# Optimization experiments

Hardware: AMD Instinct MI355X
Metric: run time of the kernel (lower is better)

Reference implementation:

```python
import jax, jax.numpy as jnp
import numpy as np


def setup_inputs() -> dict:
    key = jax.random.key(0)
    k0, k1, k2, k3, k4 = jax.random.split(key, 5)
    N, C, H, W, K = 16, 256, 32, 32, 4096
    inv = 1.0 / np.sqrt(C).astype(np.float32)
    latent = jax.random.normal(k0, (N, C, H, W), jnp.float32)
    codebook = jax.random.normal(k1, (K, C), jnp.float32) * inv
    wq = jax.random.normal(k2, (C, C), jnp.float32) * inv
    wk = jax.random.normal(k3, (C, C), jnp.float32) * inv
    wv = jax.random.normal(k4, (C, C), jnp.float32) * inv
    return {"latent": latent, "codebook": codebook, "wq": wq, "wk": wk, "wv": wv, "temperature": 1}


def reference(latent, codebook, wq, wk, wv, temperature):
    # deterministic=True, additionWeight=True, dropout=False
    # temperature >= 0 -> _gumbelAttention -> _softStraightThrough path
    assert temperature >= 0
    C = latent.shape[1]
    K = codebook.shape[0]
    scale = jnp.sqrt(jnp.asarray(C, jnp.float32))
    x = jnp.transpose(latent, (0, 2, 3, 1))          # [N,H,W,C]
    q = x @ wq.T                                      # nn.Linear: x @ W^T
    k = codebook @ wk.T                               # [K,C]
    v = codebook @ wv.T                               # [K,C]
    logit = jnp.einsum('nhwc,kc->nhwk', q, k) / scale  # [N,H,W,K]
    soft = jax.nn.softmax(logit, axis=-1)
    idx = jnp.argmax(logit, axis=-1)                  # [N,H,W]
    hard = jax.nn.one_hot(idx, K, dtype=jnp.float32)  # [N,H,W,K]
    soft_v = jnp.einsum('nhwk,kc->nhwc', soft, v)
    hard_v = jnp.einsum('nhwk,kc->nhwc', hard, v)
    # (hard - soft).detach() + soft  -> straight-through estimator
    result = jax.lax.stop_gradient(hard_v - soft_v) + soft_v
    quantized = jnp.transpose(result, (0, 3, 1, 2))   # [N,C,H,W]
    code = idx.astype(jnp.uint8)                      # sample.argmax(-1).byte()
    return (quantized, code, logit, v)
```

## Files before the change

kernel.cpp:

```cpp
#include <hip/hip_runtime.h>
#include <stdint.h>

typedef float f32x4 __attribute__((ext_vector_type(4)));
typedef short s16x8 __attribute__((ext_vector_type(8)));

#define QUANT_OFF 0
#define CODE_OFF  4194304
#define LOGIT_OFF 4210688
#define V_OFF     71319552

#define ARGMAX_MARGIN 0.0078125f

__device__ __forceinline__ unsigned short f2bf(float f) {
  unsigned int u = __float_as_uint(f);
  u = u + 0x7fffu + ((u >> 16) & 1u);
  return (unsigned short)(u >> 16);
}

__device__ __forceinline__ void load_lds16(const void* g, void* l) {
  __builtin_amdgcn_global_load_lds(
      (const __attribute__((address_space(1))) unsigned int*)g,
      (__attribute__((address_space(3))) unsigned int*)l, 16, 0, 0);
}

__global__ __launch_bounds__(256) void kvq_kernel(
    const float* __restrict__ latent, const float* __restrict__ wq,
    const float* __restrict__ cb, const float* __restrict__ wk, const float* __restrict__ wv,
    float* __restrict__ qf, unsigned short* __restrict__ qh,
    float* __restrict__ kf, unsigned short* __restrict__ kh, float* __restrict__ vout)
{
  __shared__ __align__(16) float As[64][68];
  __shared__ __align__(16) float Bs[64][68];
  const int t = threadIdx.x;
  const int bid = blockIdx.x;
  const int tx = t & 15;
  const int ry = t >> 4;

  if (bid >= 256) {
    const int qb = bid - 256;
    const int rowBase = (qb & 255) * 64;
    const int colBase = (qb >> 8) * 64;
    const int n = rowBase >> 10;
    const int hw0 = rowBase & 1023;
    const f32x4* lat4 = (const f32x4*)latent;
    const f32x4* wq4 = (const f32x4*)wq;
    float acc[4][4] = {{0.f}};
    for (int kt = 0; kt < 4; ++kt) {
      __syncthreads();
      #pragma unroll
      for (int it = 0; it < 4; ++it) {
        int c = it * 256 + t;
        int kk = c >> 4, rq = c & 15;
        f32x4 vv = lat4[(size_t)(n * 256 + kt * 64 + kk) * 256 + (hw0 >> 2) + rq];
        *(f32x4*)&As[kk][rq * 4] = vv;
      }
      #pragma unroll
      for (int it = 0; it < 4; ++it) {
        int c = it * 256 + t;
        int col = c >> 4, kq4 = c & 15;
        f32x4 vv = wq4[(size_t)(colBase + col) * 64 + kt * 16 + kq4];
        *(f32x4*)&Bs[col][kq4 * 4] = vv;
      }
      __syncthreads();
      #pragma unroll
      for (int kc = 0; kc < 16; ++kc) {
        f32x4 a[4], b[4];
        #pragma unroll
        for (int c = 0; c < 4; ++c) a[c] = *(const f32x4*)&As[kc * 4 + c][ry * 4];
        #pragma unroll
        for (int j = 0; j < 4; ++j) b[j] = *(const f32x4*)&Bs[tx + 16 * j][kc * 4];
        #pragma unroll
        for (int i = 0; i < 4; ++i)
          #pragma unroll
          for (int j = 0; j < 4; ++j) {
            acc[i][j] = fmaf(a[0][i], b[j].x, acc[i][j]);
            acc[i][j] = fmaf(a[1][i], b[j].y, acc[i][j]);
            acc[i][j] = fmaf(a[2][i], b[j].z, acc[i][j]);
            acc[i][j] = fmaf(a[3][i], b[j].w, acc[i][j]);
          }
      }
    }
    #pragma unroll
    for (int i = 0; i < 4; ++i) {
      const int r = rowBase + ry * 4 + i;
      #pragma unroll
      for (int j = 0; j < 4; ++j) {
        const int c = colBase + tx + 16 * j;
        qf[(size_t)r * 256 + c] = acc[i][j];
        qh[(size_t)r * 256 + c] = f2bf(acc[i][j] * 0.0625f);
      }
    }
  } else {
    const int rowBase = (bid & 63) * 64;
    const int colBase = (bid >> 6) * 64;
    const f32x4* cb4 = (const f32x4*)cb;
    const f32x4* wk4 = (const f32x4*)wk;
    const f32x4* wv4 = (const f32x4*)wv;
    float accK[4][4] = {{0.f}}, accV[4][4] = {{0.f}};
    for (int kt = 0; kt < 4; ++kt) {
      __syncthreads();
      #pragma unroll
      for (int it = 0; it < 4; ++it) {
        int c = it * 256 + t;
        int row = c >> 4, kq4 = c & 15;
        f32x4 vv = cb4[(size_t)(rowBase + row) * 64 + kt * 16 + kq4];
        *(f32x4*)&As[row][kq4 * 4] = vv;
      }
      #pragma unroll
      for (int it = 0; it < 4; ++it) {
        int c = it * 256 + t;
        int col = c >> 4, kq4 = c & 15;
        f32x4 vv = wk4[(size_t)(colBase + col) * 64 + kt * 16 + kq4];
        *(f32x4*)&Bs[col][kq4 * 4] = vv;
      }
      __syncthreads();
      #pragma unroll
      for (int kc = 0; kc < 16; ++kc) {
        f32x4 a[4], b[4];
        #pragma unroll
        for (int i = 0; i < 4; ++i) a[i] = *(const f32x4*)&As[ry + 16 * i][kc * 4];
        #pragma unroll
        for (int j = 0; j < 4; ++j) b[j] = *(const f32x4*)&Bs[tx + 16 * j][kc * 4];
        #pragma unroll
        for (int i = 0; i < 4; ++i)
          #pragma unroll
          for (int j = 0; j < 4; ++j) {
            accK[i][j] = fmaf(a[i].x, b[j].x, accK[i][j]);
            accK[i][j] = fmaf(a[i].y, b[j].y, accK[i][j]);
            accK[i][j] = fmaf(a[i].z, b[j].z, accK[i][j]);
            accK[i][j] = fmaf(a[i].w, b[j].w, accK[i][j]);
          }
      }
      __syncthreads();
      #pragma unroll
      for (int it = 0; it < 4; ++it) {
        int c = it * 256 + t;
        int col = c >> 4, kq4 = c & 15;
        f32x4 vv = wv4[(size_t)(colBase + col) * 64 + kt * 16 + kq4];
        *(f32x4*)&Bs[col][kq4 * 4] = vv;
      }
      __syncthreads();
      #pragma unroll
      for (int kc = 0; kc < 16; ++kc) {
        f32x4 a[4], b[4];
        #pragma unroll
        for (int i = 0; i < 4; ++i) a[i] = *(const f32x4*)&As[ry + 16 * i][kc * 4];
        #pragma unroll
        for (int j = 0; j < 4; ++j) b[j] = *(const f32x4*)&Bs[tx + 16 * j][kc * 4];
        #pragma unroll
        for (int i = 0; i < 4; ++i)
          #pragma unroll
          for (int j = 0; j < 4; ++j) {
            accV[i][j] = fmaf(a[i].x, b[j].x, accV[i][j]);
            accV[i][j] = fmaf(a[i].y, b[j].y, accV[i][j]);
            accV[i][j] = fmaf(a[i].z, b[j].z, accV[i][j]);
            accV[i][j] = fmaf(a[i].w, b[j].w, accV[i][j]);
          }
      }
    }
    #pragma unroll
    for (int i = 0; i < 4; ++i) {
      const int r = rowBase + ry + 16 * i;
      #pragma unroll
      for (int j = 0; j < 4; ++j) {
        const int c = colBase + tx + 16 * j;
        kf[(size_t)r * 256 + c] = accK[i][j];
        kh[(size_t)r * 256 + c] = f2bf(accK[i][j]);
        vout[(size_t)r * 256 + c] = accV[i][j];
      }
    }
  }
}

__global__ __launch_bounds__(256) void logit_gemm(
    const unsigned short* __restrict__ qh, const unsigned short* __restrict__ kh,
    float* __restrict__ out, float* __restrict__ pmax)
{
  __shared__ short AsBuf[2][128 * 32];
  __shared__ short BsBuf[2][128 * 32];
  __shared__ float Pm[128][2];
  const int t = threadIdx.x;
  const int bid = blockIdx.x;
  const int wg = (bid & 7) * 512 + (bid >> 3);
  const int aRow0 = (wg >> 5) * 128;
  const int bRow0 = (wg & 31) * 128;
  const int lane = t & 63, wid = t >> 6;
  const int wr = wid >> 1, wc = wid & 1;
  f32x4 acc[4][4];
  #pragma unroll
  for (int m = 0; m < 4; ++m)
    #pragma unroll
    for (int n = 0; n < 4; ++n) { acc[m][n].x = 0.f; acc[m][n].y = 0.f; acc[m][n].z = 0.f; acc[m][n].w = 0.f; }

  const short* qs = (const short*)qh;
  const short* ks = (const short*)kh;

  #define STAGE32(AB, BB, KT) do {                                          \
    _Pragma("unroll")                                                       \
    for (int ci = 0; ci < 2; ++ci) {                                        \
      int c = ci * 256 + t;                                                 \
      int row = c >> 2;                                                     \
      int slot = (c & 3) ^ (row & 3);                                       \
      int koff = (KT) * 32 + slot * 8;                                      \
      load_lds16(qs + (size_t)(aRow0 + row) * 256 + koff, (AB) + c * 8);    \
      load_lds16(ks + (size_t)(bRow0 + row) * 256 + koff, (BB) + c * 8);    \
    } } while (0)

  STAGE32(AsBuf[0], BsBuf[0], 0);
  #pragma unroll
  for (int kt = 0; kt < 8; ++kt) {
    const int buf = kt & 1;
    __syncthreads();
    if (kt < 7) STAGE32(AsBuf[buf ^ 1], BsBuf[buf ^ 1], kt + 1);
    const short* As = AsBuf[buf];
    const short* Bs = BsBuf[buf];
    s16x8 af[4], bfr[4];
    #pragma unroll
    for (int m = 0; m < 4; ++m) {
      int row = wr * 64 + m * 16 + (lane & 15);
      int slot = (lane >> 4) ^ (row & 3);
      af[m] = *(const s16x8*)(As + row * 32 + slot * 8);
    }
    #pragma unroll
    for (int n = 0; n < 4; ++n) {
      int row = wc * 64 + n * 16 + (lane & 15);
      int slot = (lane >> 4) ^ (row & 3);
      bfr[n] = *(const s16x8*)(Bs + row * 32 + slot * 8);
    }
    #pragma unroll
    for (int m = 0; m < 4; ++m)
      #pragma unroll
      for (int n = 0; n < 4; ++n)
        acc[m][n] = __builtin_amdgcn_mfma_f32_16x16x32_bf16(af[m], bfr[n], acc[m][n], 0, 0, 0);
  }
  #undef STAGE32

  #pragma unroll
  for (int m = 0; m < 4; ++m)
    #pragma unroll
    for (int j = 0; j < 4; ++j) {
      float bm = fmaxf(fmaxf(acc[m][0][j], acc[m][1][j]),
                       fmaxf(acc[m][2][j], acc[m][3][j]));
      #pragma unroll
      for (int off = 1; off < 16; off <<= 1) bm = fmaxf(bm, __shfl_xor(bm, off));
      if ((lane & 15) == 0) Pm[wr * 64 + m * 16 + (lane >> 4) * 4 + j][wc] = bm;
    }
  const int colLane = lane & 15, rowQuad = (lane >> 4) * 4;
  #pragma unroll
  for (int m = 0; m < 4; ++m)
    #pragma unroll
    for (int n = 0; n < 4; ++n) {
      int row = aRow0 + wr * 64 + m * 16 + rowQuad;
      int col = bRow0 + wc * 64 + n * 16 + colLane;
      #pragma unroll
      for (int j = 0; j < 4; ++j)
        out[(size_t)(row + j) * 4096 + col] = acc[m][n][j];
    }
  __syncthreads();
  if (t < 128) pmax[(size_t)(aRow0 + t) * 32 + (bRow0 >> 7)] = fmaxf(Pm[t][0], Pm[t][1]);
}

__global__ __launch_bounds__(1024) void finalize_kernel(
    const float* __restrict__ logit, const float* __restrict__ pmax,
    const float* __restrict__ qf, const float* __restrict__ kf,
    const float* __restrict__ vout, float* __restrict__ quant, float* __restrict__ code)
{
  __shared__ __align__(16) float Vs[32][260];
  __shared__ int idxArr[32];
  const int t = threadIdx.x, wave = t >> 6, lane = t & 63;
  const int nh = blockIdx.x, n = nh >> 5, h = nh & 31;
  for (int ri = 0; ri < 2; ++ri) {
    const int w = wave * 2 + ri;
    const size_t r = (size_t)nh * 32 + w;
    float pv = -3e38f;
    if (lane < 32) pv = pmax[r * 32 + lane];
    float gmax = pv;
    #pragma unroll
    for (int off = 32; off; off >>= 1) gmax = fmaxf(gmax, __shfl_xor(gmax, off));
    const float thr = gmax - ARGMAX_MARGIN;
    const unsigned long long bmAll = __ballot(pv >= thr);
    int tot = 0, firstJ = 0x7fffffff;
    {
      unsigned long long bm = bmAll;
      #pragma unroll 1
      while (bm) {
        const int nb = __ffsll(bm) - 1; bm &= bm - 1;
        const float2 lv = *(const float2*)&logit[r * 4096 + nb * 128 + lane * 2];
        unsigned long long c0 = __ballot(lv.x >= thr);
        unsigned long long c1 = __ballot(lv.y >= thr);
        tot += __popcll(c0) + __popcll(c1);
        if (firstJ == 0x7fffffff && (c0 | c1)) {
          int j0 = c0 ? nb * 128 + 2 * (__ffsll(c0) - 1)     : 0x7fffffff;
          int j1 = c1 ? nb * 128 + 2 * (__ffsll(c1) - 1) + 1 : 0x7fffffff;
          firstJ = j0 < j1 ? j0 : j1;
        }
      }
    }
    int bestJ = firstJ;
    if (tot > 1) {
      const f32x4 qv = ((const f32x4*)(qf + r * 256))[lane];
      float bestV = -3e38f; bestJ = 0x7fffffff;
      unsigned long long bm = bmAll;
      #pragma unroll 1
      while (bm) {
        const int nb = __ffsll(bm) - 1; bm &= bm - 1;
        const float2 lv = *(const float2*)&logit[r * 4096 + nb * 128 + lane * 2];
        unsigned long long c0 = __ballot(lv.x >= thr);
        unsigned long long c1 = __ballot(lv.y >= thr);
        #pragma unroll 1
        for (int half = 0; half < 2; ++half) {
          unsigned long long mm = half ? c1 : c0;
          #pragma unroll 1
          while (mm) {
            const int L = __ffsll(mm) - 1; mm &= mm - 1;
            const int j = nb * 128 + L * 2 + half;
            const f32x4 kv = ((const f32x4*)(kf + (size_t)j * 256))[lane];
            double s = (double)qv.x * kv.x + (double)qv.y * kv.y
                     + (double)qv.z * kv.z + (double)qv.w * kv.w;
            #pragma unroll
            for (int off = 32; off; off >>= 1) s += __shfl_xor(s, off);
            const float val = (float)(s * 0.0625);
            if (val > bestV || (val == bestV && j < bestJ)) { bestV = val; bestJ = j; }
          }
        }
      }
    }
    if (lane == 0) idxArr[w] = bestJ;
  }
  __syncthreads();
  for (int ri = 0; ri < 2; ++ri) {
    const int w2 = wave * 2 + ri;
    const int idx = idxArr[w2];
    const f32x4 vv = ((const f32x4*)(vout + (size_t)idx * 256))[lane];
    *(f32x4*)&Vs[w2][lane * 4] = vv;
  }
  __syncthreads();
  const int wcol = t & 31, cg = t >> 5;
  #pragma unroll
  for (int cc = 0; cc < 8; ++cc) {
    const int c = cg * 8 + cc;
    quant[(((size_t)n * 256 + c) * 32 + h) * 32 + wcol] = Vs[wcol][c];
  }
  if (t < 32) code[nh * 32 + t] = (float)(idxArr[t] & 255);
}

extern "C" void kernel_launch(void* const* d_in, const int* in_sizes, int n_in,
                              void* d_out, int out_size, void* d_ws, size_t ws_size,
                              hipStream_t stream) {
  (void)in_sizes; (void)n_in; (void)out_size; (void)ws_size;
  const float* latent = (const float*)d_in[0];
  const float* cb     = (const float*)d_in[1];
  const float* wq     = (const float*)d_in[2];
  const float* wk     = (const float*)d_in[3];
  const float* wv     = (const float*)d_in[4];

  float* out   = (float*)d_out;
  float* quant = out + QUANT_OFF;
  float* code  = out + CODE_OFF;
  float* logit = out + LOGIT_OFF;
  float* vout  = out + V_OFF;

  char* ws = (char*)d_ws;
  float*          qf   = (float*)(ws + 0);
  float*          kf   = (float*)(ws + 16777216);
  unsigned short* qh   = (unsigned short*)(ws + 20971520);
  unsigned short* kh   = (unsigned short*)(ws + 29360128);
  float*          pmax = (float*)(ws + 31457280);

  kvq_kernel<<<1280, 256, 0, stream>>>(latent, wq, cb, wk, wv, qf, qh, kf, kh, vout);
  logit_gemm<<<4096, 256, 0, stream>>>(qh, kh, logit, pmax);
  finalize_kernel<<<512, 1024, 0, stream>>>(logit, pmax, qf, kf, vout, quant, code);
}
```

Baseline: 170.4 us.

## Double-buffer projection GEMM tiles via direct global-to-LDS loads and split K/V blocks

Rewrites the fp32 projection kernel to stage 32-wide k-tiles with global_load_lds into double-buffered LDS, prefetching the next tile while computing on the current one. B and codebook tiles use an XOR swizzle to avoid bank conflicts. The K and V projections now run in separate blocks (512 instead of 256), which adds parallelism but loads the codebook tile twice. This kernel is a small part of the total next to the logit GEMM and finalize, so the overall effect is probably limited.

```diff
diff --git a/kernel.cpp b/kernel.cpp
--- a/kernel.cpp
+++ b/kernel.cpp
@@ -29,46 +29,52 @@
     float* __restrict__ qf, unsigned short* __restrict__ qh,
     float* __restrict__ kf, unsigned short* __restrict__ kh, float* __restrict__ vout)
 {
-  __shared__ __align__(16) float As[64][68];
-  __shared__ __align__(16) float Bs[64][68];
+  __shared__ __align__(16) float A_s[2][2048];
+  __shared__ __align__(16) float B_s[2][2048];
   const int t = threadIdx.x;
   const int bid = blockIdx.x;
   const int tx = t & 15;
   const int ry = t >> 4;
 
-  if (bid >= 256) {
-    const int qb = bid - 256;
+  if (bid >= 512) {
+    const int qb = bid - 512;
     const int rowBase = (qb & 255) * 64;
     const int colBase = (qb >> 8) * 64;
     const int n = rowBase >> 10;
     const int hw0 = rowBase & 1023;
-    const f32x4* lat4 = (const f32x4*)latent;
-    const f32x4* wq4 = (const f32x4*)wq;
     float acc[4][4] = {{0.f}};
-    for (int kt = 0; kt < 4; ++kt) {
+
+    #define QSTAGE(B, KT) do {                                                        \
+      _Pragma("unroll")                                                               \
+      for (int it = 0; it < 2; ++it) {                                                \
+        int c = it * 256 + t;                                                         \
+        int kk = c >> 4, rq = c & 15;                                                 \
+        load_lds16(latent + ((size_t)(n * 256 + (KT) * 32 + kk) * 1024 + hw0 + rq * 4), \
+                   &A_s[B][c * 4]);                                                   \
+        int col = c >> 3, ls = c & 7;                                                 \
+        int sk = ls ^ (col & 7);                                                      \
+        load_lds16(wq + ((size_t)(colBase + col) * 256 + (KT) * 32 + sk * 4),          \
+                   &B_s[B][c * 4]);                                                   \
+      } } while (0)
+
+    QSTAGE(0, 0);
+    #pragma unroll 1
+    for (int kt = 0; kt < 8; ++kt) {
+      const int buf = kt & 1;
       __syncthreads();
-      #pragma unroll
-      for (int it = 0; it < 4; ++it) {
-        int c = it * 256 + t;
-        int kk = c >> 4, rq = c & 15;
-        f32x4 vv = lat4[(size_t)(n * 256 + kt * 64 + kk) * 256 + (hw0 >> 2) + rq];
-        *(f32x4*)&As[kk][rq * 4] = vv;
-      }
-      #pragma unroll
-      for (int it = 0; it < 4; ++it) {
-        int c = it * 256 + t;
-        int col = c >> 4, kq4 = c & 15;
-        f32x4 vv = wq4[(size_t)(colBase + col) * 64 + kt * 16 + kq4];
-        *(f32x4*)&Bs[col][kq4 * 4] = vv;
-      }
-      __syncthreads();
-      #pragma unroll
-      for (int kc = 0; kc < 16; ++kc) {
+      if (kt < 7) QSTAGE(buf ^ 1, kt + 1);
+      const float* As = A_s[buf];
+      const float* Bs = B_s[buf];
+      #pragma unroll
+      for (int kc = 0; kc < 8; ++kc) {
         f32x4 a[4], b[4];
         #pragma unroll
-        for (int c = 0; c < 4; ++c) a[c] = *(const f32x4*)&As[kc * 4 + c][ry * 4];
-        #pragma unroll
-        for (int j = 0; j < 4; ++j) b[j] = *(const f32x4*)&Bs[tx + 16 * j][kc * 4];
+        for (int c = 0; c < 4; ++c) a[c] = *(const f32x4*)&As[(kc * 4 + c) * 64 + ry * 4];
+        #pragma unroll
+        for (int j = 0; j < 4; ++j) {
+          const int col = tx + 16 * j;
+          b[j] = *(const f32x4*)&Bs[col * 32 + (kc ^ (col & 7)) * 4];
+        }
         #pragma unroll
         for (int i = 0; i < 4; ++i)
           #pragma unroll
@@ -80,6 +86,7 @@
           }
       }
     }
+    #undef QSTAGE
     #pragma unroll
     for (int i = 0; i < 4; ++i) {
       const int r = rowBase + ry * 4 + i;
@@ -91,82 +98,70 @@
       }
     }
   } else {
-    const int rowBase = (bid & 63) * 64;
-    const int colBase = (bid >> 6) * 64;
-    const f32x4* cb4 = (const f32x4*)cb;
-    const f32x4* wk4 = (const f32x4*)wk;
-    const f32x4* wv4 = (const f32x4*)wv;
-    float accK[4][4] = {{0.f}}, accV[4][4] = {{0.f}};
-    for (int kt = 0; kt < 4; ++kt) {
+    const bool isV = bid >= 256;
+    const int kb = bid & 255;
+    const int rowBase = (kb & 63) * 64;
+    const int colBase = (kb >> 6) * 64;
+    const float* W = isV ? wv : wk;
+    float acc[4][4] = {{0.f}};
+
+    #define KSTAGE(B, KT) do {                                                        \
+      _Pragma("unroll")                                                               \
+      for (int it = 0; it < 2; ++it) {                                                \
+        int c = it * 256 + t;                                                         \
+        int row = c >> 3, ls = c & 7;                                                 \
+        int sk = ls ^ (row & 7);                                                      \
+        load_lds16(cb + ((size_t)(rowBase + row) * 256 + (KT) * 32 + sk * 4),          \
+                   &A_s[B][c * 4]);                                                   \
+        load_lds16(W  + ((size_t)(colBase + row) * 256 + (KT) * 32 + sk * 4),          \
+                   &B_s[B][c * 4]);                                                   \
+      } } while (0)
+
+    KSTAGE(0, 0);
+    #pragma unroll 1
+    for (int kt = 0; kt < 8; ++kt) {
+      const int buf = kt & 1;
       __syncthreads();
-      #pragma unroll
-      for (int it = 0; it < 4; ++it) {
-        int c = it * 256 + t;
-        int row = c >> 4, kq4 = c & 15;
-        f32x4 vv = cb4[(size_t)(rowBase + row) * 64 + kt * 16 + kq4];
-        *(f32x4*)&As[row][kq4 * 4] = vv;
-      }
-      #pragma unroll
-      for (int it = 0; it < 4; ++it) {
-        int c = it * 256 + t;
-        int col = c >> 4, kq4 = c & 15;
-        f32x4 vv = wk4[(size_t)(colBase + col) * 64 + kt * 16 + kq4];
-        *(f32x4*)&Bs[col][kq4 * 4] = vv;
-      }
-      __syncthreads();
-      #pragma unroll
-      for (int kc = 0; kc < 16; ++kc) {
+      if (kt < 7) KSTAGE(buf ^ 1, kt + 1);
+      const float* As = A_s[buf];
+      const float* Bs = B_s[buf];
+      #pragma unroll
+      for (int kc = 0; kc < 8; ++kc) {
         f32x4 a[4], b[4];
         #pragma unroll
-        for (int i = 0; i < 4; ++i) a[i] = *(const f32x4*)&As[ry + 16 * i][kc * 4];
-        #pragma unroll
-        for (int j = 0; j < 4; ++j) b[j] = *(const f32x4*)&Bs[tx + 16 * j][kc * 4];
+        for (int i = 0; i < 4; ++i) {
+          const int row = ry + 16 * i;
+          a[i] = *(const f32x4*)&As[row * 32 + (kc ^ (row & 7)) * 4];
+        }
+        #pragma unroll
+        for (int j = 0; j < 4; ++j) {
+          const int col = tx + 16 * j;
+          b[j] = *(const f32x4*)&Bs[col * 32 + (kc ^ (col & 7)) * 4];
+        }
         #pragma unroll
         for (int i = 0; i < 4; ++i)
           #pragma unroll
           for (int j = 0; j < 4; ++j) {
-            accK[i][j] = fmaf(a[i].x, b[j].x, accK[i][j]);
-            accK[i][j] = fmaf(a[i].y, b[j].y, accK[i][j]);
-            accK[i][j] = fmaf(a[i].z, b[j].z, accK[i][j]);
-            accK[i][j] = fmaf(a[i].w, b[j].w, accK[i][j]);
+            acc[i][j] = fmaf(a[i].x, b[j].x, acc[i][j]);
+            acc[i][j] = fmaf(a[i].y, b[j].y, acc[i][j]);
+            acc[i][j] = fmaf(a[i].z, b[j].z, acc[i][j]);
+            acc[i][j] = fmaf(a[i].w, b[j].w, acc[i][j]);
           }
       }
-      __syncthreads();
-      #pragma unroll
-      for (int it = 0; it < 4; ++it) {
-        int c = it * 256 + t;
-        int col = c >> 4, kq4 = c & 15;
-        f32x4 vv = wv4[(size_t)(colBase + col) * 64 + kt * 16 + kq4];
-        *(f32x4*)&Bs[col][kq4 * 4] = vv;
-      }
-      __syncthreads();
-      #pragma unroll
-      for (int kc = 0; kc < 16; ++kc) {
-        f32x4 a[4], b[4];
-        #pragma unroll
-        for (int i = 0; i < 4; ++i) a[i] = *(const f32x4*)&As[ry + 16 * i][kc * 4];
-        #pragma unroll
-        for (int j = 0; j < 4; ++j) b[j] = *(const f32x4*)&Bs[tx + 16 * j][kc * 4];
-        #pragma unroll
-        for (int i = 0; i < 4; ++i)
-          #pragma unroll
-          for (int j = 0; j < 4; ++j) {
-            accV[i][j] = fmaf(a[i].x, b[j].x, accV[i][j]);
-            accV[i][j] = fmaf(a[i].y, b[j].y, accV[i][j]);
-            accV[i][j] = fmaf(a[i].z, b[j].z, accV[i][j]);
-            accV[i][j] = fmaf(a[i].w, b[j].w, accV[i][j]);
-          }
-      }
-    }
+    }
+    #undef KSTAGE
     #pragma unroll
     for (int i = 0; i < 4; ++i) {
       const int r = rowBase + ry + 16 * i;
       #pragma unroll
       for (int j = 0; j < 4; ++j) {
         const int c = colBase + tx + 16 * j;
-        kf[(size_t)r * 256 + c] = accK[i][j];
-        kh[(size_t)r * 256 + c] = f2bf(accK[i][j]);
-        vout[(size_t)r * 256 + c] = accV[i][j];
+        if (isV) {
+          vout[(size_t)r * 256 + c] = acc[i][j];
+        } else {
+          kf[(size_t)r * 256 + c] = acc[i][j];
+          kh[(size_t)r * 256 + c] = f2bf(acc[i][j]);
+        }
       }
     }
   }
@@ -367,7 +362,7 @@
   unsigned short* kh   = (unsigned short*)(ws + 29360128);
   float*          pmax = (float*)(ws + 31457280);
 
-  kvq_kernel<<<1280, 256, 0, stream>>>(latent, wq, cb, wk, wv, qf, qh, kf, kh, vout);
+  kvq_kernel<<<1536, 256, 0, stream>>>(latent, wq, cb, wk, wv, qf, qh, kf, kh, vout);
   logit_gemm<<<4096, 256, 0, stream>>>(qh, kh, logit, pmax);
   finalize_kernel<<<512, 1024, 0, stream>>>(logit, pmax, qf, kf, vout, quant, code);
 }
```

New measurement: 170.2 us. No clear change (-0.1%).
